# Optimization experiments

Hardware: AMD Instinct MI355X
Metric: run time of the kernel (lower is better)

Reference implementation:

```python
import jax, jax.numpy as jnp
import numpy as np

H = 64; H2 = 32; B = 256; NPART = 64
NP = B * NPART          # 16384 part nodes
PER_TF = 512            # torque/force nodes per graph
NT = B * PER_TF; NF = NT
E = 262144              # edges per edge type
L = 5; T = 4            # 4 main hetero layers + 1 actor layer; 4 edge types
NEG = 0.2; EPS = 1e-5


def _seg_softmax(e, seg, n):
    # softmax over entries sharing the same segment id (along axis 0)
    m = jax.lax.stop_gradient(jax.ops.segment_max(e, seg, num_segments=n))
    ex = jnp.exp(e - m[seg])
    s = jax.ops.segment_sum(ex, seg, num_segments=n)
    return ex / s[seg]


def _gat(x_s, x_d, es, ed, Ws, Wd, a_s, a_d, b, n_dst):
    # PyG GATConv, heads=1, add_self_loops=False, bipartite (x_src, x_dst)
    hs = x_s @ Ws                      # [Ns,H]
    hd = x_d @ Wd                      # [Nd,H]
    e = jax.nn.leaky_relu((hs @ a_s)[es] + (hd @ a_d)[ed], NEG)   # [E]
    al = _seg_softmax(e, ed, n_dst)                                # attn per dst neighborhood
    return jax.ops.segment_sum(al[:, None] * hs[es], ed, num_segments=n_dst) + b


def _hetero_layer(xp, xt, xf, edges, Ws, Wd, a_s, a_d, b):
    # to_hetero(aggr='sum'): one GATConv per edge type, sum into each dst type
    (pts, ptd), (tps, tpd), (pfs, pfd), (fps, fpd) = edges
    out_t = _gat(xp, xt, pts, ptd, Ws[0], Wd[0], a_s[0], a_d[0], b[0], xt.shape[0])
    out_p = (_gat(xt, xp, tps, tpd, Ws[1], Wd[1], a_s[1], a_d[1], b[1], xp.shape[0])
             + _gat(xf, xp, fps, fpd, Ws[3], Wd[3], a_s[3], a_d[3], b[3], xp.shape[0]))
    out_f = _gat(xp, xf, pfs, pfd, Ws[2], Wd[2], a_s[2], a_d[2], b[2], xf.shape[0])
    return out_p, out_t, out_f


def _pool(x):
    # MultiAggregation([max, min, mean]); segments are uniform -> reshape
    xr = x.reshape(B, -1, x.shape[-1])
    return jnp.concatenate([xr.max(1), xr.min(1), xr.mean(1)], axis=-1)


def reference(mass, part_state, torque_x, force_x,
              e_pt_src, e_pt_dst, e_tp_src, e_tp_dst,
              e_pf_src, e_pf_dst, e_fp_src, e_fp_dst,
              batch, part_id,
              emb_parts_W, emb_state, W_src, W_dst, a_src, a_dst, b_conv,
              ln_gamma, ln_beta, out_a_W, out_a_b,
              innet_W, innet_b, full_W, full_b, outnet_W, outnet_b):
    edges = ((e_pt_src, e_pt_dst), (e_tp_src, e_tp_dst),
             (e_pf_src, e_pf_dst), (e_fp_src, e_fp_dst))
    idx = part_state[:, 0] + 2 * part_state[:, 1]
    xp = jnp.concatenate([mass @ emb_parts_W, emb_state[idx]], axis=-1)  # [NP,H]
    xt, xf = torque_x, force_x
    for l in range(4):  # main hetero GAT, ReLU between layers, none after last
        xp, xt, xf = _hetero_layer(xp, xt, xf, edges,
                                   W_src[l], W_dst[l], a_src[l], a_dst[l], b_conv[l])
        if l < 3:
            xp, xt, xf = jax.nn.relu(xp), jax.nn.relu(xt), jax.nn.relu(xf)
    # actor: 1-layer hetero GAT (no activation)
    ap, at, af = _hetero_layer(xp, xt, xf, edges,
                               W_src[4], W_dst[4], a_src[4], a_dst[4], b_conv[4])
    # node LayerNorm
    mu = ap.mean(-1, keepdims=True)
    var = ((ap - mu) ** 2).mean(-1, keepdims=True)
    ra = (ap - mu) / jnp.sqrt(var + EPS) * ln_gamma + ln_beta
    ra = ra @ out_a_W + out_a_b                         # [NP,2]
    soft = _seg_softmax(ra, batch, B)                   # softmax per graph, per channel
    actions = jnp.zeros((B, 2, NPART), dtype=ra.dtype).at[batch, :, part_id].set(soft)
    actions = actions.reshape(B, 2 * NPART)
    rep = jnp.concatenate([_pool(xp), _pool(xt), _pool(xf)], axis=1)   # [B, 9H]
    repV = jax.nn.gelu(rep @ innet_W + innet_b, approximate=False)
    repV = jax.nn.gelu(repV @ full_W + full_b, approximate=False)
    V = jnp.tanh(repV @ outnet_W + outnet_b)            # [B,1]
    return actions, V


def setup_inputs():
    key = jax.random.key(0)
    ks = iter(jax.random.split(key, 40))
    f32 = jnp.float32
    inp = {}
    inp['mass'] = jax.random.uniform(next(ks), (NP, 1), dtype=f32)
    inp['part_state'] = jax.random.randint(next(ks), (NP, 2), 0, 2, dtype=jnp.int32)
    inp['torque_x'] = jax.random.normal(next(ks), (NT, H), dtype=f32)
    inp['force_x'] = jax.random.normal(next(ks), (NF, H), dtype=f32)
    for name, n in [('e_pt_src', NP), ('e_pt_dst', NT), ('e_tp_src', NT), ('e_tp_dst', NP),
                    ('e_pf_src', NP), ('e_pf_dst', NF), ('e_fp_src', NF), ('e_fp_dst', NP)]:
        inp[name] = jax.random.randint(next(ks), (E,), 0, n, dtype=jnp.int32)
    inp['batch'] = (jnp.arange(NP) // NPART).astype(jnp.int32)
    inp['part_id'] = (jnp.arange(NP) % NPART).astype(jnp.int32)
    s = 1.0 / np.sqrt(H)
    inp['emb_parts_W'] = jax.random.normal(next(ks), (1, H2), dtype=f32)
    inp['emb_state'] = jax.random.normal(next(ks), (4, H2), dtype=f32)
    inp['W_src'] = jax.random.normal(next(ks), (L, T, H, H), dtype=f32) * s
    inp['W_dst'] = jax.random.normal(next(ks), (L, T, H, H), dtype=f32) * s
    inp['a_src'] = jax.random.normal(next(ks), (L, T, H), dtype=f32) * s
    inp['a_dst'] = jax.random.normal(next(ks), (L, T, H), dtype=f32) * s
    inp['b_conv'] = jax.random.normal(next(ks), (L, T, H), dtype=f32) * 0.01
    inp['ln_gamma'] = jnp.ones((H,), dtype=f32)
    inp['ln_beta'] = jnp.zeros((H,), dtype=f32)
    inp['out_a_W'] = jax.random.normal(next(ks), (H, 2), dtype=f32) * s
    inp['out_a_b'] = jnp.zeros((2,), dtype=f32)
    inp['innet_W'] = jax.random.normal(next(ks), (9 * H, H), dtype=f32) / np.sqrt(9.0 * H)
    inp['innet_b'] = jnp.zeros((H,), dtype=f32)
    inp['full_W'] = jax.random.normal(next(ks), (H, H), dtype=f32) * s
    inp['full_b'] = jnp.zeros((H,), dtype=f32)
    inp['outnet_W'] = jax.random.normal(next(ks), (H, 1), dtype=f32) * s
    inp['outnet_b'] = jnp.zeros((1,), dtype=f32)
    return inp
```

## Files before the change

### kernel.cpp

```cpp
#include <hip/hip_runtime.h>
#include <hip/hip_fp16.h>
#include <math.h>

#define NP_ 16384
#define NT_ 131072
#define NF_ 131072
#define E_  262144
#define B_  256
#define NDTOT 294912
#define E4_  1048576

#define D0 0
#define D1 131072
#define D2 147456
#define D3 278528
#define S0 0
#define S1 16384
#define S2 147456
#define S3 163840

typedef _Float16 h4 __attribute__((ext_vector_type(4)));

__device__ __forceinline__ float dot4(float4 a, float4 b) {
  return a.x * b.x + a.y * b.y + a.z * b.z + a.w * b.w;
}
__device__ __forceinline__ float4 h4tof4(h4 h) {
  return make_float4((float)h.x, (float)h.y, (float)h.z, (float)h.w);
}
__device__ __forceinline__ h4 f4toh4(float4 f) {
  h4 h; h.x = (_Float16)f.x; h.y = (_Float16)f.y; h.z = (_Float16)f.z; h.w = (_Float16)f.w;
  return h;
}

__device__ __forceinline__ void gather2(
    int kb0, int ke0, float ad0, const float* __restrict__ aS0, const _Float16* __restrict__ x0,
    int kb1, int ke1, float ad1, const float* __restrict__ aS1, const _Float16* __restrict__ x1,
    const int* __restrict__ sortsrc, int q, int lanebase,
    float4* __restrict__ acc0o, float* __restrict__ si0o,
    float4* __restrict__ acc1o, float* __restrict__ si1o) {
  float4 acc0 = make_float4(0.f, 0.f, 0.f, 0.f);
  float4 acc1 = make_float4(0.f, 0.f, 0.f, 0.f);
  float m0 = -3e38f, m1 = -3e38f, sum0 = 0.f, sum1 = 0.f;
  int len = max(ke0 - kb0, ke1 - kb1);
  for (int c = 0; c < len; c += 16) {
    int k0 = kb0 + c + q, k1 = kb1 + c + q;
    int v0 = k0 < ke0, v1 = k1 < ke1;
    int sx0 = v0 ? sortsrc[k0] : 0;
    int sx1 = v1 ? sortsrc[k1] : 0;
    float e0 = -3e38f, e1 = -3e38f;
    if (v0) { float t = aS0[sx0] + ad0; e0 = t > 0.f ? t : 0.2f * t; }
    if (v1) { float t = aS1[sx1] + ad1; e1 = t > 0.f ? t : 0.2f * t; }
    float cm0 = e0, cm1 = e1;
#pragma unroll
    for (int off = 1; off < 16; off <<= 1) {
      cm0 = fmaxf(cm0, __shfl_xor(cm0, off));
      cm1 = fmaxf(cm1, __shfl_xor(cm1, off));
    }
    float mn0 = fmaxf(m0, cm0), mn1 = fmaxf(m1, cm1);
    float w0 = v0 ? __expf(e0 - mn0) : 0.f;
    float w1 = v1 ? __expf(e1 - mn1) : 0.f;
    float ws0 = w0, ws1 = w1;
#pragma unroll
    for (int off = 1; off < 16; off <<= 1) {
      ws0 += __shfl_xor(ws0, off);
      ws1 += __shfl_xor(ws1, off);
    }
    float r0 = __expf(m0 - mn0), r1 = __expf(m1 - mn1);
    sum0 = sum0 * r0 + ws0;
    sum1 = sum1 * r1 + ws1;
    acc0.x *= r0; acc0.y *= r0; acc0.z *= r0; acc0.w *= r0;
    acc1.x *= r1; acc1.y *= r1; acc1.z *= r1; acc1.w *= r1;
    int cnt0 = ke0 - (kb0 + c); cnt0 = cnt0 < 0 ? 0 : (cnt0 > 16 ? 16 : cnt0);
    int cnt1 = ke1 - (kb1 + c); cnt1 = cnt1 < 0 ? 0 : (cnt1 > 16 ? 16 : cnt1);
    int cmax = max(cnt0, cnt1);
    for (int i = 0; i < cmax; i += 4) {
      float wa0 = __shfl(w0, lanebase + i, 64);
      float wa1 = __shfl(w0, lanebase + i + 1, 64);
      float wa2 = __shfl(w0, lanebase + i + 2, 64);
      float wa3 = __shfl(w0, lanebase + i + 3, 64);
      int sa0 = __shfl(sx0, lanebase + i, 64);
      int sa1 = __shfl(sx0, lanebase + i + 1, 64);
      int sa2 = __shfl(sx0, lanebase + i + 2, 64);
      int sa3 = __shfl(sx0, lanebase + i + 3, 64);
      float wb0 = __shfl(w1, lanebase + i, 64);
      float wb1 = __shfl(w1, lanebase + i + 1, 64);
      float wb2 = __shfl(w1, lanebase + i + 2, 64);
      float wb3 = __shfl(w1, lanebase + i + 3, 64);
      int sb0 = __shfl(sx1, lanebase + i, 64);
      int sb1 = __shfl(sx1, lanebase + i + 1, 64);
      int sb2 = __shfl(sx1, lanebase + i + 2, 64);
      int sb3 = __shfl(sx1, lanebase + i + 3, 64);
      float4 xa0 = h4tof4(*(const h4*)(x0 + (size_t)sa0 * 64 + q * 4));
      float4 xa1 = h4tof4(*(const h4*)(x0 + (size_t)sa1 * 64 + q * 4));
      float4 xa2 = h4tof4(*(const h4*)(x0 + (size_t)sa2 * 64 + q * 4));
      float4 xa3 = h4tof4(*(const h4*)(x0 + (size_t)sa3 * 64 + q * 4));
      float4 xb0 = h4tof4(*(const h4*)(x1 + (size_t)sb0 * 64 + q * 4));
      float4 xb1 = h4tof4(*(const h4*)(x1 + (size_t)sb1 * 64 + q * 4));
      float4 xb2 = h4tof4(*(const h4*)(x1 + (size_t)sb2 * 64 + q * 4));
      float4 xb3 = h4tof4(*(const h4*)(x1 + (size_t)sb3 * 64 + q * 4));
      acc0.x += wa0 * xa0.x + wa1 * xa1.x + wa2 * xa2.x + wa3 * xa3.x;
      acc0.y += wa0 * xa0.y + wa1 * xa1.y + wa2 * xa2.y + wa3 * xa3.y;
      acc0.z += wa0 * xa0.z + wa1 * xa1.z + wa2 * xa2.z + wa3 * xa3.z;
      acc0.w += wa0 * xa0.w + wa1 * xa1.w + wa2 * xa2.w + wa3 * xa3.w;
      acc1.x += wb0 * xb0.x + wb1 * xb1.x + wb2 * xb2.x + wb3 * xb3.x;
      acc1.y += wb0 * xb0.y + wb1 * xb1.y + wb2 * xb2.y + wb3 * xb3.y;
      acc1.z += wb0 * xb0.z + wb1 * xb1.z + wb2 * xb2.z + wb3 * xb3.z;
      acc1.w += wb0 * xb0.w + wb1 * xb1.w + wb2 * xb2.w + wb3 * xb3.w;
    }
    m0 = mn0; m1 = mn1;
  }
  *si0o = (sum0 > 0.f) ? 1.f / sum0 : 0.f;
  *si1o = (sum1 > 0.f) ? 1.f / sum1 : 0.f;
  *acc0o = acc0;
  *acc1o = acc1;
}

__device__ __forceinline__ void gather4(
    int kbA, int keA, float adA,
    int kbB, int keB, float adB,
    int kbC, int keC, float adC,
    int kbD, int keD, float adD,
    const float* __restrict__ aS, const _Float16* __restrict__ x,
    const int* __restrict__ sortsrc, int q, int lanebase,
    float4* accAo, float* siAo, float4* accBo, float* siBo,
    float4* accCo, float* siCo, float4* accDo, float* siDo) {
  float4 aA = make_float4(0.f, 0.f, 0.f, 0.f);
  float4 aB = aA, aC = aA, aDv = aA;
  float mA = -3e38f, mB = -3e38f, mC = -3e38f, mD = -3e38f;
  float sA = 0.f, sB = 0.f, sC = 0.f, sD = 0.f;
  int len = max(max(keA - kbA, keB - kbB), max(keC - kbC, keD - kbD));
  for (int c = 0; c < len; c += 16) {
    int kA = kbA + c + q, kB = kbB + c + q, kC = kbC + c + q, kD = kbD + c + q;
    int vA = kA < keA, vB = kB < keB, vC = kC < keC, vD = kD < keD;
    int iA = vA ? sortsrc[kA] : 0;
    int iB = vB ? sortsrc[kB] : 0;
    int iC = vC ? sortsrc[kC] : 0;
    int iD = vD ? sortsrc[kD] : 0;
    float eA = -3e38f, eB = -3e38f, eC = -3e38f, eD = -3e38f;
    if (vA) { float u = aS[iA] + adA; eA = u > 0.f ? u : 0.2f * u; }
    if (vB) { float u = aS[iB] + adB; eB = u > 0.f ? u : 0.2f * u; }
    if (vC) { float u = aS[iC] + adC; eC = u > 0.f ? u : 0.2f * u; }
    if (vD) { float u = aS[iD] + adD; eD = u > 0.f ? u : 0.2f * u; }
    float cA = eA, cB = eB, cC = eC, cD = eD;
#pragma unroll
    for (int off = 1; off < 16; off <<= 1) {
      cA = fmaxf(cA, __shfl_xor(cA, off));
      cB = fmaxf(cB, __shfl_xor(cB, off));
      cC = fmaxf(cC, __shfl_xor(cC, off));
      cD = fmaxf(cD, __shfl_xor(cD, off));
    }
    float nA = fmaxf(mA, cA), nB = fmaxf(mB, cB);
    float nC = fmaxf(mC, cC), nD = fmaxf(mD, cD);
    float wA = vA ? __expf(eA - nA) : 0.f;
    float wB = vB ? __expf(eB - nB) : 0.f;
    float wC = vC ? __expf(eC - nC) : 0.f;
    float wD = vD ? __expf(eD - nD) : 0.f;
    float uA = wA, uB = wB, uC = wC, uD = wD;
#pragma unroll
// ... 264 lines not shown

__global__ __launch_bounds__(256) void k_place(
    const int* __restrict__ d0, const int* __restrict__ s0,
    const int* __restrict__ d1, const int* __restrict__ s1,
    const int* __restrict__ d2, const int* __restrict__ s2,
    const int* __restrict__ d3, const int* __restrict__ s3,
    const int* __restrict__ cbase, int2* __restrict__ pairs) {
  __shared__ int cur[64];
  int b = blockIdx.x;
  int t = b >> 6, c = b & 63;
  const int* dp; const int* sp;
  if (t == 0) { dp = d0; sp = s0; }
  else if (t == 1) { dp = d1; sp = s1; }
  else if (t == 2) { dp = d2; sp = s2; }
  else { dp = d3; sp = s3; }
  int sh = (t & 1) ? 8 : 11;
  int tid = threadIdx.x;
  if (tid < 64) cur[tid] = cbase[(b << 6) + tid];
  __syncthreads();
  const int4* dp4 = (const int4*)dp + (size_t)c * 1024;
  const int4* sp4 = (const int4*)sp + (size_t)c * 1024;
  for (int i = tid; i < 1024; i += 256) {
    int4 d = dp4[i];
    int4 s = sp4[i];
    int pos;
    pos = atomicAdd(&cur[d.x >> sh], 1); pairs[pos] = make_int2(d.x, s.x);
    pos = atomicAdd(&cur[d.y >> sh], 1); pairs[pos] = make_int2(d.y, s.y);
    pos = atomicAdd(&cur[d.z >> sh], 1); pairs[pos] = make_int2(d.z, s.z);
    pos = atomicAdd(&cur[d.w >> sh], 1); pairs[pos] = make_int2(d.w, s.w);
  }
}

__global__ __launch_bounds__(256) void k_build(const int2* __restrict__ pairs,
    const int* __restrict__ granBase, int* __restrict__ rowptr,
    int* __restrict__ sortsrc) {
  __shared__ int cnt[2048];
  __shared__ int psum[256];
  int g = blockIdx.x;
  int t = g >> 6, gg = g & 63;
  int rows = (t & 1) ? 256 : 2048;
  int rowLo = gg * rows;
  int csr0;
  if (t == 0) csr0 = D0 + rowLo;
  else if (t == 1) csr0 = D1 + rowLo;
  else if (t == 2) csr0 = D2 + rowLo;
  else csr0 = D3 + rowLo;
  int eb = granBase[g], ee = granBase[g + 1];
  int tid = threadIdx.x;
  for (int i = tid; i < rows; i += 256) cnt[i] = 0;
  __syncthreads();
  for (int i = eb + tid; i < ee; i += 256) {
    int2 p = pairs[i];
    atomicAdd(&cnt[p.x - rowLo], 1);
  }
  __syncthreads();
  int per = rows >> 8;
  int b0 = tid * per;
  int s = 0;
  for (int j = 0; j < per; j++) s += cnt[b0 + j];
  psum[tid] = s;
  __syncthreads();
  for (int off = 1; off < 256; off <<= 1) {
    int x = 0; if (tid >= off) x = psum[tid - off];
    __syncthreads(); psum[tid] += x; __syncthreads();
  }
  int run = psum[tid] - s;
  for (int j = 0; j < per; j++) {
    int v = cnt[b0 + j];
    cnt[b0 + j] = run;
    rowptr[csr0 + b0 + j] = eb + run;
    run += v;
  }
  __syncthreads();
  for (int i = eb + tid; i < ee; i += 256) {
    int2 p = pairs[i];
    int pos = eb + atomicAdd(&cnt[p.x - rowLo], 1);
    sortsrc[pos] = p.y;
  }
}

__global__ __launch_bounds__(256) void k_layer(int l,
    const _Float16* __restrict__ xt_old, const _Float16* __restrict__ xf_old,
    const _Float16* __restrict__ hs0, const _Float16* __restrict__ hs2,
    const float* __restrict__ bconv,
    const int* __restrict__ rowptr, const int* __restrict__ sortsrc,
    const float* __restrict__ aSrd, const float* __restrict__ aDrd,
    float* __restrict__ aSwr, float* __restrict__ aDwr,
    const float* __restrict__ wsas, const float* __restrict__ wdad,
    float* __restrict__ agg1, float* __restrict__ agg3,
    _Float16* __restrict__ xt_new, _Float16* __restrict__ xf_new,
    int relu, int hasTf) {
  int bid = blockIdx.x;
  int tid = threadIdx.x;
  int q = tid & 15;
  int lanebase = (tid & 63) & 48;

  int isPart, pg = 0, tg = 0;
  if (!hasTf) { isPart = 1; pg = bid; }
  else {
    int g = bid / 5, r = bid - g * 5;
    if (r == 4) { isPart = 1; pg = g; }
    else        { isPart = 0; tg = g * 4 + r; }
  }

  if (isPart) {
    int n = pg * 16 + (tid >> 4);
    int row1 = D1 + n, row3 = D3 + n;
    int kb1 = rowptr[row1], ke1 = rowptr[row1 + 1];
    int kb3 = rowptr[row3], ke3 = rowptr[row3 + 1];
    float4 accA, accB; float siA, siB;
    gather2(kb1, ke1, aDrd[row1], aSrd + S1, xt_old,
            kb3, ke3, aDrd[row3], aSrd + S3, xf_old,
            sortsrc, q, lanebase, &accA, &siA, &accB, &siB);
    accA.x *= siA; accA.y *= siA; accA.z *= siA; accA.w *= siA;
    accB.x *= siB; accB.y *= siB; accB.z *= siB; accB.w *= siB;
    *(float4*)(agg1 + (size_t)n * 64 + q * 4) = accA;
    *(float4*)(agg3 + (size_t)n * 64 + q * 4) = accB;
    return;
  }

  int slot = tid >> 4;
  int isF = (tg >= 2048);
  int r0 = (isF ? tg - 2048 : tg) * 64 + slot;
  int csr = (isF ? D2 : D0) + r0;
  const _Float16* hs = isF ? hs2 : hs0;
  const float* aSseg = aSrd + (isF ? S2 : S0);
  int t = isF ? 2 : 0;

  int kbA = rowptr[csr],      keA = rowptr[csr + 1];
  int kbB = rowptr[csr + 16], keB = rowptr[csr + 17];
  int kbC = rowptr[csr + 32], keC = rowptr[csr + 33];
  int kbD = rowptr[csr + 48], keD = rowptr[csr + 49];
  float4 aA, aB, aC, aD4; float sA, sB, sC, sD;
  gather4(kbA, keA, aDrd[csr],      kbB, keB, aDrd[csr + 16],
          kbC, keC, aDrd[csr + 32], kbD, keD, aDrd[csr + 48],
          aSseg, hs, sortsrc, q, lanebase,
          &aA, &sA, &aB, &sB, &aC, &sC, &aD4, &sD);

  float4 bias = *(const float4*)(bconv + (size_t)(l * 4 + t) * 64 + q * 4);
  float4 o0, o1, o2, o3;
  o0.x = aA.x * sA + bias.x; o0.y = aA.y * sA + bias.y;
  o0.z = aA.z * sA + bias.z; o0.w = aA.w * sA + bias.w;
  o1.x = aB.x * sB + bias.x; o1.y = aB.y * sB + bias.y;
  o1.z = aB.z * sB + bias.z; o1.w = aB.w * sB + bias.w;
  o2.x = aC.x * sC + bias.x; o2.y = aC.y * sC + bias.y;
  o2.z = aC.z * sC + bias.z; o2.w = aC.w * sC + bias.w;
  o3.x = aD4.x * sD + bias.x; o3.y = aD4.y * sD + bias.y;
  o3.z = aD4.z * sD + bias.z; o3.w = aD4.w * sD + bias.w;
  if (relu) {
    o0.x = fmaxf(o0.x, 0.f); o0.y = fmaxf(o0.y, 0.f); o0.z = fmaxf(o0.z, 0.f); o0.w = fmaxf(o0.w, 0.f);
    o1.x = fmaxf(o1.x, 0.f); o1.y = fmaxf(o1.y, 0.f); o1.z = fmaxf(o1.z, 0.f); o1.w = fmaxf(o1.w, 0.f);
    o2.x = fmaxf(o2.x, 0.f); o2.y = fmaxf(o2.y, 0.f); o2.z = fmaxf(o2.z, 0.f); o2.w = fmaxf(o2.w, 0.f);
    o3.x = fmaxf(o3.x, 0.f); o3.y = fmaxf(o3.y, 0.f); o3.z = fmaxf(o3.z, 0.f); o3.w = fmaxf(o3.w, 0.f);
  }
  _Float16* xout = isF ? xf_new : xt_new;
  *(h4*)(xout + (size_t)r0 * 64 + q * 4) = f4toh4(o0);
  *(h4*)(xout + (size_t)(r0 + 16) * 64 + q * 4) = f4toh4(o1);
  *(h4*)(xout + (size_t)(r0 + 32) * 64 + q * 4) = f4toh4(o2);
  *(h4*)(xout + (size_t)(r0 + 48) * 64 + q * 4) = f4toh4(o3);

  int tsrc = isF ? 3 : 1, tdst = isF ? 2 : 0;
  float4 wsv = *(const float4*)(wsas + (size_t)((l + 1) * 4 + tsrc) * 64 + q * 4);
  float4 wdv = *(const float4*)(wdad + (size_t)((l + 1) * 4 + tdst) * 64 + q * 4);
  float pS0 = dot4(o0, wsv), pD0 = dot4(o0, wdv);
  float pS1 = dot4(o1, wsv), pD1 = dot4(o1, wdv);
  float pS2 = dot4(o2, wsv), pD2 = dot4(o2, wdv);
  float pS3 = dot4(o3, wsv), pD3 = dot4(o3, wdv);
#pragma unroll
  for (int off = 1; off < 16; off <<= 1) {
    pS0 += __shfl_xor(pS0, off); pD0 += __shfl_xor(pD0, off);
    pS1 += __shfl_xor(pS1, off); pD1 += __shfl_xor(pD1, off);
    pS2 += __shfl_xor(pS2, off); pD2 += __shfl_xor(pD2, off);
    pS3 += __shfl_xor(pS3, off); pD3 += __shfl_xor(pD3, off);
  }
  if (q == 0) {
    int sb = isF ? S3 : S1;
    int db = isF ? D2 : D0;
    aSwr[sb + r0]      = pS0; aDwr[db + r0]      = pD0;
    aSwr[sb + r0 + 16] = pS1; aDwr[db + r0 + 16] = pD1;
    aSwr[sb + r0 + 32] = pS2; aDwr[db + r0 + 32] = pD2;
    aSwr[sb + r0 + 48] = pS3; aDwr[db + r0 + 48] = pD3;
  }
}

__global__ __launch_bounds__(256) void k_xform(int l,
    const float* __restrict__ Wsrc, const float* __restrict__ bconv,
    const float* __restrict__ agg1, const float* __restrict__ agg3,
    float* __restrict__ aSwr, float* __restrict__ aDwr,
    const float* __restrict__ wsas, const float* __restrict__ wdad,
    float* __restrict__ xpo, _Float16* __restrict__ hs0n, _Float16* __restrict__ hs2n,
    int relu, int writeHs, int writeXp,
    const float* __restrict__ gamma, const float* __restrict__ beta,
    const float* __restrict__ oaW, const float* __restrict__ oab,
    float* __restrict__ raOut) {
  __shared__ float WA[4096], WB[4096];
  int tid = threadIdx.x;
  int q = tid & 15;
  int lanebase = (tid & 63) & 48;
  int n = blockIdx.x * 16 + (tid >> 4);
  {
    const float4* W1g = (const float4*)(Wsrc + (size_t)(l * 4 + 1) * 4096);
    const float4* W3g = (const float4*)(Wsrc + (size_t)(l * 4 + 3) * 4096);
#pragma unroll
    for (int i = 0; i < 4; i++) {
      ((float4*)WA)[i * 256 + tid] = W1g[i * 256 + tid];
      ((float4*)WB)[i * 256 + tid] = W3g[i * 256 + tid];
    }
  }
  float4 accA = *(const float4*)(agg1 + (size_t)n * 64 + q * 4);
  float4 accB = *(const float4*)(agg3 + (size_t)n * 64 + q * 4);
  __syncthreads();

  float4 o;
  {
    float4 b1 = *(const float4*)(bconv + (size_t)(l * 4 + 1) * 64 + q * 4);
    float4 b3 = *(const float4*)(bconv + (size_t)(l * 4 + 3) * 64 + q * 4);
    o = make_float4(b1.x + b3.x, b1.y + b3.y, b1.z + b3.z, b1.w + b3.w);
  }
  const float4* WAc = (const float4*)WA;
  const float4* WBc = (const float4*)WB;
#pragma unroll 4
  for (int k4 = 0; k4 < 16; k4++) {
    float ax = __shfl(accA.x, lanebase + k4, 64);
    float ay = __shfl(accA.y, lanebase + k4, 64);
    float az = __shfl(accA.z, lanebase + k4, 64);
    float aw = __shfl(accA.w, lanebase + k4, 64);
    float bx = __shfl(accB.x, lanebase + k4, 64);
    float by = __shfl(accB.y, lanebase + k4, 64);
    float bz = __shfl(accB.z, lanebase + k4, 64);
    float bw = __shfl(accB.w, lanebase + k4, 64);
    float4 wa0 = WAc[(k4 * 4 + 0) * 16 + q];
    float4 wa1 = WAc[(k4 * 4 + 1) * 16 + q];
    float4 wa2 = WAc[(k4 * 4 + 2) * 16 + q];
    float4 wa3 = WAc[(k4 * 4 + 3) * 16 + q];
    float4 wb0 = WBc[(k4 * 4 + 0) * 16 + q];
    float4 wb1 = WBc[(k4 * 4 + 1) * 16 + q];
    float4 wb2 = WBc[(k4 * 4 + 2) * 16 + q];
    float4 wb3 = WBc[(k4 * 4 + 3) * 16 + q];
    o.x += ax * wa0.x + ay * wa1.x + az * wa2.x + aw * wa3.x
         + bx * wb0.x + by * wb1.x + bz * wb2.x + bw * wb3.x;
    o.y += ax * wa0.y + ay * wa1.y + az * wa2.y + aw * wa3.y
         + bx * wb0.y + by * wb1.y + bz * wb2.y + bw * wb3.y;
    o.z += ax * wa0.z + ay * wa1.z + az * wa2.z + aw * wa3.z
         + bx * wb0.z + by * wb1.z + bz * wb2.z + bw * wb3.z;
    o.w += ax * wa0.w + ay * wa1.w + az * wa2.w + aw * wa3.w
         + bx * wb0.w + by * wb1.w + bz * wb2.w + bw * wb3.w;
  }

  if (raOut) {
    float ssum = o.x + o.y + o.z + o.w;
#pragma unroll
    for (int off = 1; off < 16; off <<= 1) ssum += __shfl_xor(ssum, off);
    float mean = ssum * (1.f / 64.f);
    float dx = o.x - mean, dy = o.y - mean, dz = o.z - mean, dw = o.w - mean;
    float v2 = dx * dx + dy * dy + dz * dz + dw * dw;
#pragma unroll
    for (int off = 1; off < 16; off <<= 1) v2 += __shfl_xor(v2, off);
    float rstd = 1.f / sqrtf(v2 * (1.f / 64.f) + 1e-5f);
    float4 g4 = *(const float4*)(gamma + q * 4);
    float4 be4 = *(const float4*)(beta + q * 4);
    float y0 = dx * rstd * g4.x + be4.x;
    float y1 = dy * rstd * g4.y + be4.y;
    float y2 = dz * rstd * g4.z + be4.z;
    float y3 = dw * rstd * g4.w + be4.w;
    float4 wAv = *(const float4*)(oaW + q * 8);
    float4 wBv = *(const float4*)(oaW + q * 8 + 4);
    float p0 = y0 * wAv.x + y1 * wAv.z + y2 * wBv.x + y3 * wBv.z;
    float p1 = y0 * wAv.y + y1 * wAv.w + y2 * wBv.y + y3 * wBv.w;
#pragma unroll
    for (int off = 1; off < 16; off <<= 1) {
      p0 += __shfl_xor(p0, off);
      p1 += __shfl_xor(p1, off);
    }
    if (q == 0) {
      raOut[(size_t)n * 2]     = p0 + oab[0];
      raOut[(size_t)n * 2 + 1] = p1 + oab[1];
    }
    return;
  }

  if (relu) { o.x = fmaxf(o.x, 0.f); o.y = fmaxf(o.y, 0.f); o.z = fmaxf(o.z, 0.f); o.w = fmaxf(o.w, 0.f); }
  if (writeXp) *(float4*)(xpo + (size_t)n * 64 + q * 4) = o;

  {
    float4 w0 = *(const float4*)(wsas + (size_t)((l + 1) * 4 + 0) * 64 + q * 4);
    float4 w2 = *(const float4*)(wsas + (size_t)((l + 1) * 4 + 2) * 64 + q * 4);
    float4 d1 = *(const float4*)(wdad + (size_t)((l + 1) * 4 + 1) * 64 + q * 4);
    float4 d3 = *(const float4*)(wdad + (size_t)((l + 1) * 4 + 3) * 64 + q * 4);
    float p0 = dot4(o, w0), p2 = dot4(o, w2), p1 = dot4(o, d1), p3 = dot4(o, d3);
#pragma unroll
    for (int off = 1; off < 16; off <<= 1) {
      p0 += __shfl_xor(p0, off); p2 += __shfl_xor(p2, off);
      p1 += __shfl_xor(p1, off); p3 += __shfl_xor(p3, off);
    }
    if (q == 0) { aSwr[S0 + n] = p0; aSwr[S2 + n] = p2; aDwr[D1 + n] = p1; aDwr[D3 + n] = p3; }
  }

  if (writeHs) {
    __syncthreads();
    {
      const float4* W0g = (const float4*)(Wsrc + (size_t)((l + 1) * 4 + 0) * 4096);
      const float4* W2g = (const float4*)(Wsrc + (size_t)((l + 1) * 4 + 2) * 4096);
#pragma unroll
      for (int i = 0; i < 4; i++) {
        ((float4*)WA)[i * 256 + tid] = W0g[i * 256 + tid];
        ((float4*)WB)[i * 256 + tid] = W2g[i * 256 + tid];
      }
    }
    __syncthreads();
    float4 h0 = make_float4(0.f, 0.f, 0.f, 0.f);
    float4 h2 = make_float4(0.f, 0.f, 0.f, 0.f);
#pragma unroll 4
    for (int k4 = 0; k4 < 16; k4++) {
      float ox = __shfl(o.x, lanebase + k4, 64);
      float oy = __shfl(o.y, lanebase + k4, 64);
      float oz = __shfl(o.z, lanebase + k4, 64);
      float ow = __shfl(o.w, lanebase + k4, 64);
      float4 a0 = WAc[(k4 * 4 + 0) * 16 + q];
      float4 a1 = WAc[(k4 * 4 + 1) * 16 + q];
      float4 a2 = WAc[(k4 * 4 + 2) * 16 + q];
      float4 a3 = WAc[(k4 * 4 + 3) * 16 + q];
      float4 c0 = WBc[(k4 * 4 + 0) * 16 + q];
      float4 c1 = WBc[(k4 * 4 + 1) * 16 + q];
      float4 c2 = WBc[(k4 * 4 + 2) * 16 + q];
      float4 c3 = WBc[(k4 * 4 + 3) * 16 + q];
      h0.x += ox * a0.x + oy * a1.x + oz * a2.x + ow * a3.x;
      h0.y += ox * a0.y + oy * a1.y + oz * a2.y + ow * a3.y;
      h0.z += ox * a0.z + oy * a1.z + oz * a2.z + ow * a3.z;
      h0.w += ox * a0.w + oy * a1.w + oz * a2.w + ow * a3.w;
      h2.x += ox * c0.x + oy * c1.x + oz * c2.x + ow * c3.x;
      h2.y += ox * c0.y + oy * c1.y + oz * c2.y + ow * c3.y;
      h2.z += ox * c0.z + oy * c1.z + oz * c2.z + ow * c3.z;
      h2.w += ox * c0.w + oy * c1.w + oz * c2.w + ow * c3.w;
    }
    *(h4*)(hs0n + (size_t)n * 64 + q * 4) = f4toh4(h0);
    *(h4*)(hs2n + (size_t)n * 64 + q * 4) = f4toh4(h2);
  }
}

__global__ __launch_bounds__(64) void k_actor(const float* __restrict__ ra,
                                              float* __restrict__ outp) {
  int g = blockIdx.x;
  int p = threadIdx.x;
  float2 rv = *(const float2*)(ra + (size_t)(g * 64 + p) * 2);
  float m0 = rv.x, m1 = rv.y;
  for (int off = 32; off > 0; off >>= 1) {
    m0 = fmaxf(m0, __shfl_xor(m0, off));
    m1 = fmaxf(m1, __shfl_xor(m1, off));
  }
  float e0 = __expf(rv.x - m0), e1 = __expf(rv.y - m1);
  float s0 = e0, s1 = e1;
  for (int off = 32; off > 0; off >>= 1) {
    s0 += __shfl_xor(s0, off);
    s1 += __shfl_xor(s1, off);
  }
  outp[g * 128 + p] = e0 / s0;
  outp[g * 128 + 64 + p] = e1 / s1;
}

__global__ __launch_bounds__(256) void k_pool(const float* __restrict__ xp,
    const _Float16* __restrict__ xt, const _Float16* __restrict__ xf,
    float* __restrict__ pool) {
  __shared__ float pmax[4][64], pmin[4][64], psum[4][64];
  int b = blockIdx.x;
  int g = b / 9, c = b % 9;
  int tid = threadIdx.x;
  int grp = tid >> 6, col = tid & 63;
  float mx = -3e38f, mn = 3e38f, sm = 0.f;
  if (c == 0) {
    const float* src = xp + (size_t)g * 64 * 64;
    for (int r = grp; r < 64; r += 4) {
      float v = src[(size_t)r * 64 + col];
      mx = fmaxf(mx, v); mn = fminf(mn, v); sm += v;
    }
  } else {
    const _Float16* src;
    if (c <= 4) src = xt + ((size_t)g * 512 + (size_t)(c - 1) * 128) * 64;
    else        src = xf + ((size_t)g * 512 + (size_t)(c - 5) * 128) * 64;
    for (int r = grp; r < 128; r += 4) {
      float v = (float)src[(size_t)r * 64 + col];
      mx = fmaxf(mx, v); mn = fminf(mn, v); sm += v;
    }
  }
  pmax[grp][col] = mx; pmin[grp][col] = mn; psum[grp][col] = sm;
  __syncthreads();
  if (grp == 0) {
    float M = fmaxf(fmaxf(pmax[0][col], pmax[1][col]), fmaxf(pmax[2][col], pmax[3][col]));
    float m = fminf(fminf(pmin[0][col], pmin[1][col]), fminf(pmin[2][col], pmin[3][col]));
    float S = psum[0][col] + psum[1][col] + psum[2][col] + psum[3][col];
    float* o = pool + ((size_t)(g * 9 + c) * 3) * 64;
    o[col] = M; o[64 + col] = m; o[128 + col] = S;
  }
}

__global__ __launch_bounds__(256) void k_vhead(const float* __restrict__ pool,
    const float* __restrict__ inW, const float* __restrict__ inb,
    const float* __restrict__ fW, const float* __restrict__ fb,
    const float* __restrict__ oW, const float* __restrict__ ob,
    float* __restrict__ outV) {
  __shared__ float rep[576];
  __shared__ float red[256];
  __shared__ float h1[64];
  int g = blockIdx.x, tid = threadIdx.x;
  if (tid < 64) {
    int col = tid;
    const float* pg = pool + (size_t)g * 9 * 3 * 64;
    rep[col] = pg[col];
    rep[64 + col] = pg[64 + col];
    rep[128 + col] = pg[128 + col] * (1.f / 64.f);
    float M = -3e38f, m = 3e38f, S = 0.f;
    for (int c = 1; c <= 4; c++) {
      const float* p = pg + (size_t)c * 192;
      M = fmaxf(M, p[col]); m = fminf(m, p[64 + col]); S += p[128 + col];
    }
    rep[192 + col] = M; rep[256 + col] = m; rep[320 + col] = S * (1.f / 512.f);
    M = -3e38f; m = 3e38f; S = 0.f;
    for (int c = 5; c <= 8; c++) {
      const float* p = pg + (size_t)c * 192;
      M = fmaxf(M, p[col]); m = fminf(m, p[64 + col]); S += p[128 + col];
// ... 9 lines not shown
    red[tid] = s;
  }
  __syncthreads();
  if (tid < 64) {
    float s = red[tid] + red[64 + tid] + red[128 + tid] + red[192 + tid] + inb[tid];
    h1[tid] = 0.5f * s * (1.f + erff(s * ISQ2));
  }
  __syncthreads();
  if (tid < 64) {
    float s = fb[tid];
    for (int k = 0; k < 64; k++) s += h1[k] * fW[k * 64 + tid];
    float h2 = 0.5f * s * (1.f + erff(s * ISQ2));
    float p = h2 * oW[tid];
    for (int off = 32; off > 0; off >>= 1) p += __shfl_xor(p, off);
    if (tid == 0) outV[g] = tanhf(p + ob[0]);
  }
}

extern "C" void kernel_launch(void* const* d_in, const int* in_sizes, int n_in,
                              void* d_out, int out_size, void* d_ws, size_t ws_size,
                              hipStream_t stream) {
  (void)in_sizes; (void)n_in; (void)out_size; (void)ws_size;
  const float* mass = (const float*)d_in[0];
  const int*   ps   = (const int*)d_in[1];
  const float* torque_x = (const float*)d_in[2];
  const float* force_x  = (const float*)d_in[3];
  const int* ept_s = (const int*)d_in[4];  const int* ept_d = (const int*)d_in[5];
  const int* etp_s = (const int*)d_in[6];  const int* etp_d = (const int*)d_in[7];
  const int* epf_s = (const int*)d_in[8];  const int* epf_d = (const int*)d_in[9];
  const int* efp_s = (const int*)d_in[10]; const int* efp_d = (const int*)d_in[11];
  const float* embW  = (const float*)d_in[14];
  const float* embS  = (const float*)d_in[15];
  const float* Wsrc  = (const float*)d_in[16];
  const float* Wdst  = (const float*)d_in[17];
  const float* asrc  = (const float*)d_in[18];
  const float* adst  = (const float*)d_in[19];
  const float* bconv = (const float*)d_in[20];
  const float* gamma = (const float*)d_in[21];
  const float* beta  = (const float*)d_in[22];
  const float* oaW   = (const float*)d_in[23];
  const float* oab   = (const float*)d_in[24];
  const float* inW   = (const float*)d_in[25];
  const float* inb   = (const float*)d_in[26];
  const float* fW    = (const float*)d_in[27];
  const float* fb    = (const float*)d_in[28];
  const float* oW    = (const float*)d_in[29];
  const float* ob    = (const float*)d_in[30];

  char* base = (char*)d_ws;
  size_t off = 0;
  auto alloc = [&](size_t bytes) -> void* {
    void* r = base + off;
    off = (off + bytes + 255) & ~(size_t)255;
    return r;
  };
  float* xp  = (float*)alloc((size_t)NP_ * 64 * 4);
  _Float16* xtb[2]; _Float16* xfb[2];
  xtb[0] = (_Float16*)alloc((size_t)NT_ * 64 * 2);
  xtb[1] = (_Float16*)alloc((size_t)NT_ * 64 * 2);
  xfb[0] = (_Float16*)alloc((size_t)NF_ * 64 * 2);
  xfb[1] = (_Float16*)alloc((size_t)NF_ * 64 * 2);
  _Float16* xth = (_Float16*)alloc((size_t)NT_ * 64 * 2);
  _Float16* xfh = (_Float16*)alloc((size_t)NF_ * 64 * 2);
  _Float16* hs0b[2]; _Float16* hs2b[2];
  hs0b[0] = (_Float16*)alloc((size_t)NP_ * 64 * 2);
  hs0b[1] = (_Float16*)alloc((size_t)NP_ * 64 * 2);
  hs2b[0] = (_Float16*)alloc((size_t)NP_ * 64 * 2);
  hs2b[1] = (_Float16*)alloc((size_t)NP_ * 64 * 2);
  float* aSb[2], *aDb[2];
  aSb[0] = (float*)alloc((size_t)NDTOT * 4);
  aSb[1] = (float*)alloc((size_t)NDTOT * 4);
  aDb[0] = (float*)alloc((size_t)NDTOT * 4);
  aDb[1] = (float*)alloc((size_t)NDTOT * 4);
  float* wsas = (float*)alloc(1280 * 4);
  float* wdad = (float*)alloc(1280 * 4);
  float* pool = (float*)alloc((size_t)B_ * 9 * 3 * 64 * 4);
  float* ra   = (float*)alloc((size_t)NP_ * 2 * 4);
  int* rowptr = (int*)alloc((size_t)(NDTOT + 1) * 4);
  int* sortsrc = (int*)alloc((size_t)E4_ * 4);
  int2* pairs  = (int2*)alloc((size_t)E4_ * 8);
  int* counts  = (int*)alloc(16384 * 4);
  int* cbase   = (int*)alloc(16384 * 4);
  int* granBase = (int*)alloc(257 * 4);
  float* agg1 = (float*)pairs;
  float* agg3 = agg1 + (size_t)NP_ * 64;

  k_wa<<<40, 64, 0, stream>>>(Wsrc, Wdst, asrc, adst, wsas, wdad);
  k_build_xp<<<NP_ / 16, 256, 0, stream>>>(mass, ps, embW, embS, Wsrc, wsas, wdad,
                                           hs0b[0], hs2b[0], aSb[0], aDb[0]);
  k_init_dots<<<(NT_ + NF_) / 16, 256, 0, stream>>>(torque_x, force_x,
                                                    wsas, wdad, aSb[0], aDb[0],
                                                    xth, xfh);
  k_count<<<256, 256, 0, stream>>>(ept_d, etp_d, epf_d, efp_d, counts);
  k_bases<<<1, 256, 0, stream>>>(counts, cbase, granBase, rowptr);
  k_place<<<256, 256, 0, stream>>>(ept_d, ept_s, etp_d, etp_s, epf_d, epf_s,
                                   efp_d, efp_s, cbase, pairs);
  k_build<<<256, 256, 0, stream>>>(pairs, granBase, rowptr, sortsrc);

  for (int l = 0; l < 5; l++) {
    int ri = l & 1, wi = (l + 1) & 1;
    int relu = (l < 3) ? 1 : 0;
    const _Float16* xt_old = (l == 0) ? xth : xtb[(l + 1) & 1];
    const _Float16* xf_old = (l == 0) ? xfh : xfb[(l + 1) & 1];
    _Float16* xt_new = xtb[l & 1];
    _Float16* xf_new = xfb[l & 1];
    int hasTf = (l < 4) ? 1 : 0;
    int grid = hasTf ? (NP_ / 16 + (NT_ + NF_) / 64) : (NP_ / 16);
    k_layer<<<grid, 256, 0, stream>>>(l, xt_old, xf_old,
                                      hs0b[l & 1], hs2b[l & 1], bconv,
                                      rowptr, sortsrc,
                                      aSb[ri], aDb[ri], aSb[wi], aDb[wi],
                                      wsas, wdad, agg1, agg3,
                                      xt_new, xf_new, relu, hasTf);
    k_xform<<<NP_ / 16, 256, 0, stream>>>(l, Wsrc, bconv, agg1, agg3,
                                          aSb[wi], aDb[wi], wsas, wdad,
                                          xp, hs0b[(l + 1) & 1], hs2b[(l + 1) & 1],
                                          relu, (l < 3) ? 1 : 0, (l == 3) ? 1 : 0,
                                          gamma, beta, oaW, oab,
                                          (l == 4) ? ra : (float*)nullptr);
  }

  float* outp = (float*)d_out;
  k_actor<<<B_, 64, 0, stream>>>(ra, outp);
  k_pool<<<B_ * 9, 256, 0, stream>>>(xp, xtb[1], xfb[1], pool);
  k_vhead<<<B_, 256, 0, stream>>>(pool, inW, inb, fW, fb, oW, ob, outp + B_ * 128);
}
```

Baseline: 550.4 us.

## Fuse part-node transform into layer kernel and fully unroll gather2 inner loop

Part-node blocks of k_layer now do the work k_xform used to do, in the same block. They load the W1/W3 weights into shared memory, apply the dense transform, LayerNorm or actor head, the next-layer attention dots and the hs projections. This removes one kernel launch per layer and the round trip of the agg1/agg3 intermediates through global memory. The cost is a static 32KB shared allocation on every k_layer block, including torque/force blocks that never touch it, which may lower occupancy for the gather-heavy blocks. Separately, the gather2 chunk loop is fully unrolled to 16 edges instead of stopping at the valid count, so it relies on out-of-range weights being zero and their source indices being safe to load.

New measurement: 570.8 us. 3.7% more time.

```diff
diff --git a/kernel.cpp b/kernel.cpp
--- a/kernel.cpp
+++ b/kernel.cpp
@@ -70,10 +70,8 @@
     sum1 = sum1 * r1 + ws1;
     acc0.x *= r0; acc0.y *= r0; acc0.z *= r0; acc0.w *= r0;
     acc1.x *= r1; acc1.y *= r1; acc1.z *= r1; acc1.w *= r1;
-    int cnt0 = ke0 - (kb0 + c); cnt0 = cnt0 < 0 ? 0 : (cnt0 > 16 ? 16 : cnt0);
-    int cnt1 = ke1 - (kb1 + c); cnt1 = cnt1 < 0 ? 0 : (cnt1 > 16 ? 16 : cnt1);
-    int cmax = max(cnt0, cnt1);
-    for (int i = 0; i < cmax; i += 4) {
+#pragma unroll
+    for (int i = 0; i < 16; i += 4) {
       float wa0 = __shfl(w0, lanebase + i, 64);
       float wa1 = __shfl(w0, lanebase + i + 1, 64);
       float wa2 = __shfl(w0, lanebase + i + 2, 64);
@@ -504,14 +502,18 @@
 __global__ __launch_bounds__(256) void k_layer(int l,
     const _Float16* __restrict__ xt_old, const _Float16* __restrict__ xf_old,
     const _Float16* __restrict__ hs0, const _Float16* __restrict__ hs2,
-    const float* __restrict__ bconv,
+    const float* __restrict__ Wsrc, const float* __restrict__ bconv,
     const int* __restrict__ rowptr, const int* __restrict__ sortsrc,
     const float* __restrict__ aSrd, const float* __restrict__ aDrd,
     float* __restrict__ aSwr, float* __restrict__ aDwr,
     const float* __restrict__ wsas, const float* __restrict__ wdad,
-    float* __restrict__ agg1, float* __restrict__ agg3,
+    float* __restrict__ xpo, _Float16* __restrict__ hs0n, _Float16* __restrict__ hs2n,
     _Float16* __restrict__ xt_new, _Float16* __restrict__ xf_new,
-    int relu, int hasTf) {
+    int relu, int hasTf, int writeHs, int writeXp,
+    const float* __restrict__ gamma, const float* __restrict__ beta,
+    const float* __restrict__ oaW, const float* __restrict__ oab,
+    float* __restrict__ raOut) {
+  __shared__ float WA[4096], WB[4096];
   int bid = blockIdx.x;
   int tid = threadIdx.x;
   int q = tid & 15;
@@ -526,6 +528,15 @@
   }
 
   if (isPart) {
+    {
+      const float4* W1g = (const float4*)(Wsrc + (size_t)(l * 4 + 1) * 4096);
+      const float4* W3g = (const float4*)(Wsrc + (size_t)(l * 4 + 3) * 4096);
+#pragma unroll
+      for (int i = 0; i < 4; i++) {
+        ((float4*)WA)[i * 256 + tid] = W1g[i * 256 + tid];
+        ((float4*)WB)[i * 256 + tid] = W3g[i * 256 + tid];
+      }
+    }
     int n = pg * 16 + (tid >> 4);
     int row1 = D1 + n, row3 = D3 + n;
     int kb1 = rowptr[row1], ke1 = rowptr[row1 + 1];
@@ -536,8 +547,133 @@
             sortsrc, q, lanebase, &accA, &siA, &accB, &siB);
     accA.x *= siA; accA.y *= siA; accA.z *= siA; accA.w *= siA;
     accB.x *= siB; accB.y *= siB; accB.z *= siB; accB.w *= siB;
-    *(float4*)(agg1 + (size_t)n * 64 + q * 4) = accA;
-    *(float4*)(agg3 + (size_t)n * 64 + q * 4) = accB;
+    __syncthreads();
+
+    float4 o;
+    {
+      float4 b1 = *(const float4*)(bconv + (size_t)(l * 4 + 1) * 64 + q * 4);
+      float4 b3 = *(const float4*)(bconv + (size_t)(l * 4 + 3) * 64 + q * 4);
+      o = make_float4(b1.x + b3.x, b1.y + b3.y, b1.z + b3.z, b1.w + b3.w);
+    }
+    const float4* WAc = (const float4*)WA;
+    const float4* WBc = (const float4*)WB;
+#pragma unroll 4
+    for (int k4 = 0; k4 < 16; k4++) {
+      float ax = __shfl(accA.x, lanebase + k4, 64);
+      float ay = __shfl(accA.y, lanebase + k4, 64);
+      float az = __shfl(accA.z, lanebase + k4, 64);
+      float aw = __shfl(accA.w, lanebase + k4, 64);
+      float bx = __shfl(accB.x, lanebase + k4, 64);
+      float by = __shfl(accB.y, lanebase + k4, 64);
+      float bz = __shfl(accB.z, lanebase + k4, 64);
+      float bw = __shfl(accB.w, lanebase + k4, 64);
+      float4 wa0 = WAc[(k4 * 4 + 0) * 16 + q];
+      float4 wa1 = WAc[(k4 * 4 + 1) * 16 + q];
+      float4 wa2 = WAc[(k4 * 4 + 2) * 16 + q];
+      float4 wa3 = WAc[(k4 * 4 + 3) * 16 + q];
+      float4 wb0 = WBc[(k4 * 4 + 0) * 16 + q];
+      float4 wb1 = WBc[(k4 * 4 + 1) * 16 + q];
+      float4 wb2 = WBc[(k4 * 4 + 2) * 16 + q];
+      float4 wb3 = WBc[(k4 * 4 + 3) * 16 + q];
+      o.x += ax * wa0.x + ay * wa1.x + az * wa2.x + aw * wa3.x
+           + bx * wb0.x + by * wb1.x + bz * wb2.x + bw * wb3.x;
+      o.y += ax * wa0.y + ay * wa1.y + az * wa2.y + aw * wa3.y
+           + bx * wb0.y + by * wb1.y + bz * wb2.y + bw * wb3.y;
+      o.z += ax * wa0.z + ay * wa1.z + az * wa2.z + aw * wa3.z
+           + bx * wb0.z + by * wb1.z + bz * wb2.z + bw * wb3.z;
+      o.w += ax * wa0.w + ay * wa1.w + az * wa2.w + aw * wa3.w
+           + bx * wb0.w + by * wb1.w + bz * wb2.w + bw * wb3.w;
+    }
+
+    if (raOut) {
+      float ssum = o.x + o.y + o.z + o.w;
+#pragma unroll
+      for (int off = 1; off < 16; off <<= 1) ssum += __shfl_xor(ssum, off);
+      float mean = ssum * (1.f / 64.f);
+      float dx = o.x - mean, dy = o.y - mean, dz = o.z - mean, dw = o.w - mean;
+      float v2 = dx * dx + dy * dy + dz * dz + dw * dw;
+#pragma unroll
+      for (int off = 1; off < 16; off <<= 1) v2 += __shfl_xor(v2, off);
+      float rstd = 1.f / sqrtf(v2 * (1.f / 64.f) + 1e-5f);
+      float4 g4 = *(const float4*)(gamma + q * 4);
+      float4 be4 = *(const float4*)(beta + q * 4);
+      float y0 = dx * rstd * g4.x + be4.x;
+      float y1 = dy * rstd * g4.y + be4.y;
+      float y2 = dz * rstd * g4.z + be4.z;
+      float y3 = dw * rstd * g4.w + be4.w;
+      float4 wAv = *(const float4*)(oaW + q * 8);
+      float4 wBv = *(const float4*)(oaW + q * 8 + 4);
+      float p0 = y0 * wAv.x + y1 * wAv.z + y2 * wBv.x + y3 * wBv.z;
+      float p1 = y0 * wAv.y + y1 * wAv.w + y2 * wBv.y + y3 * wBv.w;
+#pragma unroll
+      for (int off = 1; off < 16; off <<= 1) {
+        p0 += __shfl_xor(p0, off);
+        p1 += __shfl_xor(p1, off);
+      }
+      if (q == 0) {
+        raOut[(size_t)n * 2]     = p0 + oab[0];
+        raOut[(size_t)n * 2 + 1] = p1 + oab[1];
+      }
+      return;
+    }
+
+    if (relu) { o.x = fmaxf(o.x, 0.f); o.y = fmaxf(o.y, 0.f); o.z = fmaxf(o.z, 0.f); o.w = fmaxf(o.w, 0.f); }
+    if (writeXp) *(float4*)(xpo + (size_t)n * 64 + q * 4) = o;
+
+    {
+      float4 w0 = *(const float4*)(wsas + (size_t)((l + 1) * 4 + 0) * 64 + q * 4);
+      float4 w2 = *(const float4*)(wsas + (size_t)((l + 1) * 4 + 2) * 64 + q * 4);
+      float4 d1 = *(const float4*)(wdad + (size_t)((l + 1) * 4 + 1) * 64 + q * 4);
+      float4 d3 = *(const float4*)(wdad + (size_t)((l + 1) * 4 + 3) * 64 + q * 4);
+      float p0 = dot4(o, w0), p2 = dot4(o, w2), p1 = dot4(o, d1), p3 = dot4(o, d3);
+#pragma unroll
+      for (int off = 1; off < 16; off <<= 1) {
+        p0 += __shfl_xor(p0, off); p2 += __shfl_xor(p2, off);
+        p1 += __shfl_xor(p1, off); p3 += __shfl_xor(p3, off);
+      }
+      if (q == 0) { aSwr[S0 + n] = p0; aSwr[S2 + n] = p2; aDwr[D1 + n] = p1; aDwr[D3 + n] = p3; }
+    }
+
+    if (writeHs) {
+      __syncthreads();
+      {
+        const float4* W0g = (const float4*)(Wsrc + (size_t)((l + 1) * 4 + 0) * 4096);
+        const float4* W2g = (const float4*)(Wsrc + (size_t)((l + 1) * 4 + 2) * 4096);
+#pragma unroll
+        for (int i = 0; i < 4; i++) {
+          ((float4*)WA)[i * 256 + tid] = W0g[i * 256 + tid];
+          ((float4*)WB)[i * 256 + tid] = W2g[i * 256 + tid];
+        }
+      }
+      __syncthreads();
+      float4 h0 = make_float4(0.f, 0.f, 0.f, 0.f);
+      float4 h2 = make_float4(0.f, 0.f, 0.f, 0.f);
+#pragma unroll 4
+      for (int k4 = 0; k4 < 16; k4++) {
+        float ox = __shfl(o.x, lanebase + k4, 64);
+        float oy = __shfl(o.y, lanebase + k4, 64);
+        float oz = __shfl(o.z, lanebase + k4, 64);
+        float ow = __shfl(o.w, lanebase + k4, 64);
+        float4 a0 = WAc[(k4 * 4 + 0) * 16 + q];
+        float4 a1 = WAc[(k4 * 4 + 1) * 16 + q];
+        float4 a2 = WAc[(k4 * 4 + 2) * 16 + q];
+        float4 a3 = WAc[(k4 * 4 + 3) * 16 + q];
+        float4 c0 = WBc[(k4 * 4 + 0) * 16 + q];
+        float4 c1 = WBc[(k4 * 4 + 1) * 16 + q];
+        float4 c2 = WBc[(k4 * 4 + 2) * 16 + q];
+        float4 c3 = WBc[(k4 * 4 + 3) * 16 + q];
+        h0.x += ox * a0.x + oy * a1.x + oz * a2.x + ow * a3.x;
+        h0.y += ox * a0.y + oy * a1.y + oz * a2.y + ow * a3.y;
+        h0.z += ox * a0.z + oy * a1.z + oz * a2.z + ow * a3.z;
+        h0.w += ox * a0.w + oy * a1.w + oz * a2.w + ow * a3.w;
+        h2.x += ox * c0.x + oy * c1.x + oz * c2.x + ow * c3.x;
+        h2.y += ox * c0.y + oy * c1.y + oz * c2.y + ow * c3.y;
+        h2.z += ox * c0.z + oy * c1.z + oz * c2.z + ow * c3.z;
+        h2.w += ox * c0.w + oy * c1.w + oz * c2.w + ow * c3.w;
+      }
+      *(h4*)(hs0n + (size_t)n * 64 + q * 4) = f4toh4(h0);
+      *(h4*)(hs2n + (size_t)n * 64 + q * 4) = f4toh4(h2);
+    }
     return;
   }
 
@@ -602,161 +738,6 @@
     aSwr[sb + r0 + 16] = pS1; aDwr[db + r0 + 16] = pD1;
     aSwr[sb + r0 + 32] = pS2; aDwr[db + r0 + 32] = pD2;
     aSwr[sb + r0 + 48] = pS3; aDwr[db + r0 + 48] = pD3;
-  }
-}
-
-__global__ __launch_bounds__(256) void k_xform(int l,
-    const float* __restrict__ Wsrc, const float* __restrict__ bconv,
-    const float* __restrict__ agg1, const float* __restrict__ agg3,
-    float* __restrict__ aSwr, float* __restrict__ aDwr,
-    const float* __restrict__ wsas, const float* __restrict__ wdad,
-    float* __restrict__ xpo, _Float16* __restrict__ hs0n, _Float16* __restrict__ hs2n,
-    int relu, int writeHs, int writeXp,
-    const float* __restrict__ gamma, const float* __restrict__ beta,
-    const float* __restrict__ oaW, const float* __restrict__ oab,
-    float* __restrict__ raOut) {
-  __shared__ float WA[4096], WB[4096];
-  int tid = threadIdx.x;
-  int q = tid & 15;
-  int lanebase = (tid & 63) & 48;
-  int n = blockIdx.x * 16 + (tid >> 4);
-  {
-    const float4* W1g = (const float4*)(Wsrc + (size_t)(l * 4 + 1) * 4096);
-    const float4* W3g = (const float4*)(Wsrc + (size_t)(l * 4 + 3) * 4096);
-#pragma unroll
-    for (int i = 0; i < 4; i++) {
-      ((float4*)WA)[i * 256 + tid] = W1g[i * 256 + tid];
-      ((float4*)WB)[i * 256 + tid] = W3g[i * 256 + tid];
-    }
-  }
-  float4 accA = *(const float4*)(agg1 + (size_t)n * 64 + q * 4);
-  float4 accB = *(const float4*)(agg3 + (size_t)n * 64 + q * 4);
-  __syncthreads();
-
-  float4 o;
-  {
-    float4 b1 = *(const float4*)(bconv + (size_t)(l * 4 + 1) * 64 + q * 4);
-    float4 b3 = *(const float4*)(bconv + (size_t)(l * 4 + 3) * 64 + q * 4);
-    o = make_float4(b1.x + b3.x, b1.y + b3.y, b1.z + b3.z, b1.w + b3.w);
-  }
-  const float4* WAc = (const float4*)WA;
-  const float4* WBc = (const float4*)WB;
-#pragma unroll 4
-  for (int k4 = 0; k4 < 16; k4++) {
-    float ax = __shfl(accA.x, lanebase + k4, 64);
-    float ay = __shfl(accA.y, lanebase + k4, 64);
-    float az = __shfl(accA.z, lanebase + k4, 64);
-    float aw = __shfl(accA.w, lanebase + k4, 64);
-    float bx = __shfl(accB.x, lanebase + k4, 64);
-    float by = __shfl(accB.y, lanebase + k4, 64);
-    float bz = __shfl(accB.z, lanebase + k4, 64);
-    float bw = __shfl(accB.w, lanebase + k4, 64);
-    float4 wa0 = WAc[(k4 * 4 + 0) * 16 + q];
-    float4 wa1 = WAc[(k4 * 4 + 1) * 16 + q];
-    float4 wa2 = WAc[(k4 * 4 + 2) * 16 + q];
-    float4 wa3 = WAc[(k4 * 4 + 3) * 16 + q];
-    float4 wb0 = WBc[(k4 * 4 + 0) * 16 + q];
-    float4 wb1 = WBc[(k4 * 4 + 1) * 16 + q];
-    float4 wb2 = WBc[(k4 * 4 + 2) * 16 + q];
-    float4 wb3 = WBc[(k4 * 4 + 3) * 16 + q];
-    o.x += ax * wa0.x + ay * wa1.x + az * wa2.x + aw * wa3.x
-         + bx * wb0.x + by * wb1.x + bz * wb2.x + bw * wb3.x;
-    o.y += ax * wa0.y + ay * wa1.y + az * wa2.y + aw * wa3.y
-         + bx * wb0.y + by * wb1.y + bz * wb2.y + bw * wb3.y;
-    o.z += ax * wa0.z + ay * wa1.z + az * wa2.z + aw * wa3.z
-         + bx * wb0.z + by * wb1.z + bz * wb2.z + bw * wb3.z;
-    o.w += ax * wa0.w + ay * wa1.w + az * wa2.w + aw * wa3.w
-         + bx * wb0.w + by * wb1.w + bz * wb2.w + bw * wb3.w;
-  }
-
-  if (raOut) {
-    float ssum = o.x + o.y + o.z + o.w;
-#pragma unroll
-    for (int off = 1; off < 16; off <<= 1) ssum += __shfl_xor(ssum, off);
-    float mean = ssum * (1.f / 64.f);
-    float dx = o.x - mean, dy = o.y - mean, dz = o.z - mean, dw = o.w - mean;
-    float v2 = dx * dx + dy * dy + dz * dz + dw * dw;
-#pragma unroll
-    for (int off = 1; off < 16; off <<= 1) v2 += __shfl_xor(v2, off);
-    float rstd = 1.f / sqrtf(v2 * (1.f / 64.f) + 1e-5f);
-    float4 g4 = *(const float4*)(gamma + q * 4);
-    float4 be4 = *(const float4*)(beta + q * 4);
-    float y0 = dx * rstd * g4.x + be4.x;
-    float y1 = dy * rstd * g4.y + be4.y;
-    float y2 = dz * rstd * g4.z + be4.z;
-    float y3 = dw * rstd * g4.w + be4.w;
-    float4 wAv = *(const float4*)(oaW + q * 8);
-    float4 wBv = *(const float4*)(oaW + q * 8 + 4);
-    float p0 = y0 * wAv.x + y1 * wAv.z + y2 * wBv.x + y3 * wBv.z;
-    float p1 = y0 * wAv.y + y1 * wAv.w + y2 * wBv.y + y3 * wBv.w;
-#pragma unroll
-    for (int off = 1; off < 16; off <<= 1) {
-      p0 += __shfl_xor(p0, off);
-      p1 += __shfl_xor(p1, off);
-    }
-    if (q == 0) {
-      raOut[(size_t)n * 2]     = p0 + oab[0];
-      raOut[(size_t)n * 2 + 1] = p1 + oab[1];
-    }
-    return;
-  }
-
-  if (relu) { o.x = fmaxf(o.x, 0.f); o.y = fmaxf(o.y, 0.f); o.z = fmaxf(o.z, 0.f); o.w = fmaxf(o.w, 0.f); }
-  if (writeXp) *(float4*)(xpo + (size_t)n * 64 + q * 4) = o;
-
-  {
-    float4 w0 = *(const float4*)(wsas + (size_t)((l + 1) * 4 + 0) * 64 + q * 4);
-    float4 w2 = *(const float4*)(wsas + (size_t)((l + 1) * 4 + 2) * 64 + q * 4);
-    float4 d1 = *(const float4*)(wdad + (size_t)((l + 1) * 4 + 1) * 64 + q * 4);
-    float4 d3 = *(const float4*)(wdad + (size_t)((l + 1) * 4 + 3) * 64 + q * 4);
-    float p0 = dot4(o, w0), p2 = dot4(o, w2), p1 = dot4(o, d1), p3 = dot4(o, d3);
-#pragma unroll
-    for (int off = 1; off < 16; off <<= 1) {
-      p0 += __shfl_xor(p0, off); p2 += __shfl_xor(p2, off);
-      p1 += __shfl_xor(p1, off); p3 += __shfl_xor(p3, off);
-    }
-    if (q == 0) { aSwr[S0 + n] = p0; aSwr[S2 + n] = p2; aDwr[D1 + n] = p1; aDwr[D3 + n] = p3; }
-  }
-
-  if (writeHs) {
-    __syncthreads();
-    {
-      const float4* W0g = (const float4*)(Wsrc + (size_t)((l + 1) * 4 + 0) * 4096);
-      const float4* W2g = (const float4*)(Wsrc + (size_t)((l + 1) * 4 + 2) * 4096);
-#pragma unroll
-      for (int i = 0; i < 4; i++) {
-        ((float4*)WA)[i * 256 + tid] = W0g[i * 256 + tid];
-        ((float4*)WB)[i * 256 + tid] = W2g[i * 256 + tid];
-      }
-    }
-    __syncthreads();
-    float4 h0 = make_float4(0.f, 0.f, 0.f, 0.f);
-    float4 h2 = make_float4(0.f, 0.f, 0.f, 0.f);
-#pragma unroll 4
-    for (int k4 = 0; k4 < 16; k4++) {
-      float ox = __shfl(o.x, lanebase + k4, 64);
-      float oy = __shfl(o.y, lanebase + k4, 64);
-      float oz = __shfl(o.z, lanebase + k4, 64);
-      float ow = __shfl(o.w, lanebase + k4, 64);
-      float4 a0 = WAc[(k4 * 4 + 0) * 16 + q];
-      float4 a1 = WAc[(k4 * 4 + 1) * 16 + q];
-      float4 a2 = WAc[(k4 * 4 + 2) * 16 + q];
-      float4 a3 = WAc[(k4 * 4 + 3) * 16 + q];
-      float4 c0 = WBc[(k4 * 4 + 0) * 16 + q];
-      float4 c1 = WBc[(k4 * 4 + 1) * 16 + q];
-      float4 c2 = WBc[(k4 * 4 + 2) * 16 + q];
-      float4 c3 = WBc[(k4 * 4 + 3) * 16 + q];
-      h0.x += ox * a0.x + oy * a1.x + oz * a2.x + ow * a3.x;
-      h0.y += ox * a0.y + oy * a1.y + oz * a2.y + ow * a3.y;
-      h0.z += ox * a0.z + oy * a1.z + oz * a2.z + ow * a3.z;
-      h0.w += ox * a0.w + oy * a1.w + oz * a2.w + ow * a3.w;
-      h2.x += ox * c0.x + oy * c1.x + oz * c2.x + ow * c3.x;
-      h2.y += ox * c0.y + oy * c1.y + oz * c2.y + ow * c3.y;
-      h2.z += ox * c0.z + oy * c1.z + oz * c2.z + ow * c3.z;
-      h2.w += ox * c0.w + oy * c1.w + oz * c2.w + ow * c3.w;
-    }
-    *(h4*)(hs0n + (size_t)n * 64 + q * 4) = f4toh4(h0);
-    *(h4*)(hs2n + (size_t)n * 64 + q * 4) = f4toh4(h2);
   }
 }
 
@@ -932,8 +913,6 @@
   int* counts  = (int*)alloc(16384 * 4);
   int* cbase   = (int*)alloc(16384 * 4);
   int* granBase = (int*)alloc(257 * 4);
-  float* agg1 = (float*)pairs;
-  float* agg3 = agg1 + (size_t)NP_ * 64;
 
   k_wa<<<40, 64, 0, stream>>>(Wsrc, Wdst, asrc, adst, wsas, wdad);
   k_build_xp<<<NP_ / 16, 256, 0, stream>>>(mass, ps, embW, embS, Wsrc, wsas, wdad,
@@ -957,17 +936,15 @@
     int hasTf = (l < 4) ? 1 : 0;
     int grid = hasTf ? (NP_ / 16 + (NT_ + NF_) / 64) : (NP_ / 16);
     k_layer<<<grid, 256, 0, stream>>>(l, xt_old, xf_old,
-                                      hs0b[l & 1], hs2b[l & 1], bconv,
+                                      hs0b[l & 1], hs2b[l & 1], Wsrc, bconv,
                                       rowptr, sortsrc,
                                       aSb[ri], aDb[ri], aSb[wi], aDb[wi],
-                                      wsas, wdad, agg1, agg3,
-                                      xt_new, xf_new, relu, hasTf);
-    k_xform<<<NP_ / 16, 256, 0, stream>>>(l, Wsrc, bconv, agg1, agg3,
-                                          aSb[wi], aDb[wi], wsas, wdad,
-                                          xp, hs0b[(l + 1) & 1], hs2b[(l + 1) & 1],
-                                          relu, (l < 3) ? 1 : 0, (l == 3) ? 1 : 0,
-                                          gamma, beta, oaW, oab,
-                                          (l == 4) ? ra : (float*)nullptr);
+                                      wsas, wdad,
+                                      xp, hs0b[(l + 1) & 1], hs2b[(l + 1) & 1],
+                                      xt_new, xf_new,
+                                      relu, hasTf, (l < 3) ? 1 : 0, (l == 3) ? 1 : 0,
+                                      gamma, beta, oaW, oab,
+                                      (l == 4) ? ra : (float*)nullptr);
   }
 
   float* outp = (float*)d_out;
```
